# Performance work log

Hardware: AMD Instinct MI355X
Metric: run time of the kernel (lower is better)

## Reference

```python
import jax, jax.numpy as jnp
import numpy as np

HIDDEN = 256
OUT_CH = 3
OMEGA_0 = 30.0
PATCH = 5


def setup_inputs() -> dict:
    key = jax.random.key(0)
    ks = jax.random.split(key, 9)
    B, C, H, W = 1, 128, 256, 256
    in_dim = C * PATCH * PATCH + 2  # 3202
    xi = jax.random.normal(ks[0], (B, C, H, W), dtype=jnp.float32)

    def lin(kw, kb, fi, fo):
        s = 1.0 / np.sqrt(fi)
        Wm = jax.random.uniform(kw, (fi, fo), jnp.float32, -s, s)
        bm = jax.random.uniform(kb, (fo,), jnp.float32, -s, s)
        return Wm, bm

    W1, b1 = lin(ks[1], ks[2], in_dim, HIDDEN)
    W2, b2 = lin(ks[3], ks[4], HIDDEN, HIDDEN)
    W3, b3 = lin(ks[5], ks[6], HIDDEN, HIDDEN)
    W4, b4 = lin(ks[7], ks[8], HIDDEN, OUT_CH)
    return {"xi": xi, "W1": W1, "b1": b1, "W2": W2, "b2": b2,
            "W3": W3, "b3": b3, "W4": W4, "b4": b4}


def _make_coords(B, H, W, dtype):
    # normalized pixel coords in [-1, 1], shape [B*H*W, 2]
    ys = jnp.linspace(-1.0, 1.0, H, dtype=dtype)
    xs = jnp.linspace(-1.0, 1.0, W, dtype=dtype)
    gy, gx = jnp.meshgrid(ys, xs, indexing="ij")
    coords = jnp.stack([gy, gx], axis=-1).reshape(H * W, 2)
    return jnp.tile(coords, (B, 1))


def reference(xi, W1, b1, W2, b2, W3, b3, W4, b4):
    B, C, H, W = xi.shape
    # im2col 5x5 patch gather (zero pad), like F.unfold with padding=2
    patches = jax.lax.conv_general_dilated_patches(
        xi, (PATCH, PATCH), (1, 1), "SAME")  # [B, C*25, H, W]
    feat = jnp.transpose(patches, (0, 2, 3, 1)).reshape(B * H * W, C * PATCH * PATCH)
    coords = _make_coords(B, H, W, xi.dtype)
    x = jnp.concatenate([feat, coords], axis=-1)  # [N, 3202]
    h = jnp.sin(OMEGA_0 * (x @ W1 + b1))
    h = jnp.sin(OMEGA_0 * (h @ W2 + b2))
    h = jnp.sin(OMEGA_0 * (h @ W3 + b3))
    out = h @ W4 + b4  # [N, 3]
    rgb = out.reshape(B, H, W, OUT_CH).transpose(0, 3, 1, 2)
    return rgb
```

## Files before the change

kernel.cpp:

```cpp
#include <hip/hip_runtime.h>
#include <math.h>
#include <stdint.h>

typedef _Float16 f16;
typedef _Float16 f16x8 __attribute__((ext_vector_type(8)));
typedef float f32x4 __attribute__((ext_vector_type(4)));
typedef unsigned short u16;
typedef u16 u16x8 __attribute__((ext_vector_type(8)));

#define HID 256
#define NS1C 100
#define NS2 8
#define NPX 65536
#define BPXG 256
#define NBG (NPX/BPXG)
#define SPAD 260
#define NSP (SPAD*SPAD)

#define OFF_W1C 0
#define SZ_W1C  ((size_t)NS1C*32768)
#define OFF_W2  SZ_W1C
#define SZ_W2   ((size_t)NS2*32768)
#define OFF_W3  (OFF_W2+SZ_W2)
#define OFF_XH  ((size_t)4194304)
#define SZ_XP   ((size_t)NSP*128*2)
#define OFF_XL  (OFF_XH + SZ_XP)
#define OFF_HH  (OFF_XL + SZ_XP)
#define SZ_HP   ((size_t)NPX*HID*2)
#define OFF_HL  (OFF_HH + SZ_HP)

__device__ static const int TAPOFF25[25] = {
  0*SPAD+0, 0*SPAD+1, 0*SPAD+2, 0*SPAD+3, 0*SPAD+4,
  1*SPAD+0, 1*SPAD+1, 1*SPAD+2, 1*SPAD+3, 1*SPAD+4,
  2*SPAD+0, 2*SPAD+1, 2*SPAD+2, 2*SPAD+3, 2*SPAD+4,
  3*SPAD+0, 3*SPAD+1, 3*SPAD+2, 3*SPAD+3, 3*SPAD+4,
  4*SPAD+0, 4*SPAD+1, 4*SPAD+2, 4*SPAD+3, 4*SPAD+4
};

__device__ inline void split2(float v, u16& h, u16& l){
  f16 hv = (f16)v;
  f16 lv = (f16)(v - (float)hv);
  h = __builtin_bit_cast(u16, hv);
  l = __builtin_bit_cast(u16, lv);
}

__device__ inline void prep_w_body(const float* __restrict__ W, int Kact,
                                   u16* __restrict__ outp, int t){
  int s = t >> 10, r = t & 1023;
  int w = r >> 8, nf = (r >> 6) & 3, l = r & 63;
  int col = w*64 + nf*16 + (l & 15);
  int kb  = s*32 + (l >> 4)*8;
  u16x8 hv, lv;
  #pragma unroll
  for (int j = 0; j < 8; ++j){
    int k = kb + j;
    float v = (k < Kact) ? W[(size_t)k*HID + col] : 0.f;
    u16 h, lo; split2(v, h, lo);
    hv[j] = h; lv[j] = lo;
  }
  size_t U0 = ((((size_t)s*4 + w)*4 + nf)*2 + 0)*64 + l;
  *(u16x8*)(outp + U0*8)      = hv;
  *(u16x8*)(outp + (U0+64)*8) = lv;
}

__device__ inline void prep_w1c_body(const float* __restrict__ W1,
                                     u16* __restrict__ outp, int t){
  int s = t >> 10, r = t & 1023;
  int w = r >> 8, nf = (r >> 6) & 3, l = r & 63;
  int col = w*64 + nf*16 + (l & 15);
  int tap = s >> 2, cg = s & 3;
  int cb  = cg*32 + (l >> 4)*8;
  u16x8 hv, lv;
  #pragma unroll
  for (int j = 0; j < 8; ++j){
    int c = cb + j;
    float v = W1[(size_t)(c*25 + tap)*HID + col];
    u16 h, lo; split2(v, h, lo);
    hv[j] = h; lv[j] = lo;
  }
  size_t U0 = ((((size_t)s*4 + w)*4 + nf)*2 + 0)*64 + l;
  *(u16x8*)(outp + U0*8)      = hv;
  *(u16x8*)(outp + (U0+64)*8) = lv;
}

__device__ inline void prep_x_body(const float* __restrict__ xi,
                                   u16* __restrict__ Xh, u16* __restrict__ Xl,
                                   int sp){
  if (sp >= NSP) return;
  int py = sp / SPAD;
  int px = sp - py*SPAD;
  bool inb = (py >= 2) & (py < 258) & (px >= 2) & (px < 258);
  const float* xin = xi + ((size_t)(py-2)<<8) + (px-2);
  #pragma unroll 4
  for (int cg = 0; cg < 16; ++cg){
    u16x8 hv, lv;
    #pragma unroll
    for (int j = 0; j < 8; ++j){
      float v = inb ? xin[((size_t)(cg*8 + j))<<16] : 0.f;
      u16 h, l; split2(v, h, l); hv[j] = h; lv[j] = l;
    }
    *(u16x8*)(Xh + (size_t)sp*128 + cg*8) = hv;
    *(u16x8*)(Xl + (size_t)sp*128 + cg*8) = lv;
  }
}

__global__ __launch_bounds__(256)
void prep_all(const float* __restrict__ xi, const float* __restrict__ W1,
              const float* __restrict__ W2, const float* __restrict__ W3,
              u16* __restrict__ W1c, u16* __restrict__ W2p, u16* __restrict__ W3p,
              u16* __restrict__ Xh, u16* __restrict__ Xl){
  int bid = blockIdx.x, tid = threadIdx.x;
  if (bid < 400){
    prep_w1c_body(W1, W1c, bid*256 + tid);
  } else if (bid < 432){
    prep_w_body(W2, HID, W2p, (bid-400)*256 + tid);
  } else if (bid < 464){
    prep_w_body(W3, HID, W3p, (bid-432)*256 + tid);
  } else {
    prep_x_body(xi, Xh, Xl, (bid-464)*256 + tid);
  }
}

template<int MODE>
__global__ __launch_bounds__(512, 2)
void gemm(const u16* __restrict__ Ah, const u16* __restrict__ Al,
          const u16* __restrict__ Wp, const float* __restrict__ W1,
          const float* __restrict__ bias, u16* __restrict__ Hh, u16* __restrict__ Hl,
          const float* __restrict__ W4, const float* __restrict__ b4,
          float* __restrict__ out, int nt)
{
  __shared__ __align__(16) u16 Sb[65536];

  const int tid  = threadIdx.x;
  const int lane = tid & 63;
  const int wv   = tid >> 6;
  const int wm   = wv >> 2, wn = wv & 3;

  int bid = blockIdx.x;
  bid = (bid & 7)*(NBG/8) + (bid >> 3);
  const int pxb = bid * BPXG;
  const int y   = bid;

  const int ybase  = y*SPAD;
  const int alane  = (lane & 15);
  const int akoff  = (lane >> 4)*8;
  const size_t abase0 = MODE == 0
      ? ((size_t)(ybase + wv*32 + alane)*128 + akoff)
      : ((size_t)(pxb + wv*32 + alane)*HID + akoff);
  const size_t abaseStride = MODE == 0 ? (size_t)16*128 : (size_t)16*HID;

  f32x4 acc[8][4];
  #pragma unroll
  for (int a=0;a<8;a++)
    #pragma unroll
    for (int bq=0;bq<4;bq++) acc[a][bq] = f32x4{0.f,0.f,0.f,0.f};

#define A_STAGE(S, BUF) do { \
    size_t soff; \
    if (MODE == 0){ \
      const int tap = (S) >> 2, cg = (S) & 3; \
      soff = abase0 + (size_t)TAPOFF25[tap]*128 + cg*32; \
    } else { \
      soff = abase0 + (size_t)(S)*32; \
    } \
    _Pragma("unroll") \
    for (int u=0;u<2;++u){ \
      const int mfb = wv*2 + u; \
      const size_t off = soff + (size_t)u*abaseStride; \
      __builtin_amdgcn_global_load_lds( \
        (const __attribute__((address_space(1))) uint32_t*)(Ah + off), \
        (__attribute__((address_space(3))) uint32_t*)((char*)Sb + (size_t)(BUF)*32768 + (mfb*2+0)*1024), \
        16, 0, 0); \
      __builtin_amdgcn_global_load_lds( \
        (const __attribute__((address_space(1))) uint32_t*)(Al + off), \
        (__attribute__((address_space(3))) uint32_t*)((char*)Sb + (size_t)(BUF)*32768 + (mfb*2+1)*1024), \
        16, 0, 0); \
    } \
  } while(0)

#define B_STAGE(S, BUF) do { \
    const char* _src = (const char*)Wp + (size_t)(S)*32768 + wv*4096 + lane*16; \
    char* _dst = (char*)Sb + 65536 + (size_t)(BUF)*32768 + wv*4096; \
    _Pragma("unroll") \
    for (int i=0;i<4;++i) \
      __builtin_amdgcn_global_load_lds( \
        (const __attribute__((address_space(1))) uint32_t*)(_src + i*1024), \
        (__attribute__((address_space(3))) uint32_t*)(_dst + i*1024), 16, 0, 0); \
  } while(0)

  A_STAGE(0, 0); B_STAGE(0, 0);

  for (int t = 0; t < nt; ++t){
    asm volatile("s_waitcnt vmcnt(0)" ::: "memory");
    __builtin_amdgcn_s_barrier();
    __builtin_amdgcn_sched_barrier(0);
    const int cur = t & 1;

    const u16* Abuf = (const u16*)Sb + (size_t)cur*16384;
    const u16* Bbuf = (const u16*)Sb + 32768 + (size_t)cur*16384;

    f16x8 bh[4], bl[4];
    #pragma unroll
    for (int nf=0;nf<4;++nf){
      bh[nf] = *(const f16x8*)(Bbuf + ((size_t)((wn*4+nf)*2+0)*64 + lane)*8);
      bl[nf] = *(const f16x8*)(Bbuf + ((size_t)((wn*4+nf)*2+1)*64 + lane)*8);
    }
    __builtin_amdgcn_sched_barrier(0);
    if (t+1 < nt){
      A_STAGE(t+1, cur^1);
      B_STAGE(t+1, cur^1);
    }

    __builtin_amdgcn_s_setprio(1);
    #pragma unroll
    for (int hf=0; hf<2; ++hf){
      f16x8 ahv[4], alv[4];
      #pragma unroll
      for (int m=0;m<4;++m){
        const int mfb = wm*8 + hf*4 + m;
        ahv[m] = *(const f16x8*)(Abuf + ((size_t)(mfb*2+0)*64 + lane)*8);
        alv[m] = *(const f16x8*)(Abuf + ((size_t)(mfb*2+1)*64 + lane)*8);
      }
      #pragma unroll
      for (int m=0;m<4;++m)
        #pragma unroll
        for (int nf=0;nf<4;++nf)
          acc[hf*4+m][nf] = __builtin_amdgcn_mfma_f32_16x16x32_f16(ahv[m], bh[nf], acc[hf*4+m][nf], 0,0,0);
      #pragma unroll
      for (int m=0;m<4;++m)
        #pragma unroll
        for (int nf=0;nf<4;++nf)
          acc[hf*4+m][nf] = __builtin_amdgcn_mfma_f32_16x16x32_f16(alv[m], bh[nf], acc[hf*4+m][nf], 0,0,0);
      #pragma unroll
      for (int m=0;m<4;++m)
        #pragma unroll
        for (int nf=0;nf<4;++nf)
          acc[hf*4+m][nf] = __builtin_amdgcn_mfma_f32_16x16x32_f16(ahv[m], bl[nf], acc[hf*4+m][nf], 0,0,0);
    }
    __builtin_amdgcn_s_setprio(0);
  }

  __syncthreads();

  float bcol[4];
  #pragma unroll
  for (int nf=0;nf<4;++nf) bcol[nf] = bias[wn*64 + nf*16 + (lane&15)];

  if (MODE == 0){
    float wyv[4], wxv[4];
    #pragma unroll
    for (int nf=0;nf<4;++nf){
      int col = wn*64 + nf*16 + (lane&15);
      wyv[nf] = W1[(size_t)3200*HID + col];
      wxv[nf] = W1[(size_t)3201*HID + col];
    }
    const float gy = -1.f + (2.f/255.f)*(float)y;
    #pragma unroll
    for (int mf=0;mf<8;++mf)
      #pragma unroll
      for (int nf=0;nf<4;++nf)
        #pragma unroll
        for (int j=0;j<4;++j){
          int row = wm*128 + mf*16 + (lane>>4)*4 + j;
          float gx = -1.f + (2.f/255.f)*(float)row;
          float z = acc[mf][nf][j] + bcol[nf] + gy*wyv[nf] + gx*wxv[nf];
          float h = sinf(30.f*z);
          u16 hh,ll; split2(h,hh,ll);
          int col = wn*64 + nf*16 + (lane&15);
          size_t o = (size_t)(pxb+row)*HID + col;
          Hh[o] = hh; Hl[o] = ll;
        }
  } else if (MODE == 1){
    #pragma unroll
    for (int mf=0;mf<8;++mf)
      #pragma unroll
      for (int nf=0;nf<4;++nf)
        #pragma unroll
        for (int j=0;j<4;++j){
          float z = acc[mf][nf][j] + bcol[nf];
          float h = sinf(30.f*z);
          u16 hh,ll; split2(h,hh,ll);
          int row = wm*128 + mf*16 + (lane>>4)*4 + j;
          int col = wn*64 + nf*16 + (lane&15);
          size_t o = (size_t)(pxb+row)*HID + col;
          Hh[o] = hh; Hl[o] = ll;
        }
  } else {
    float (*red)[BPXG][3] = (float(*)[BPXG][3])(void*)Sb;
    float w4v[4][3];
    #pragma unroll
    for (int nf=0;nf<4;++nf){
      int col = wn*64 + nf*16 + (lane&15);
      w4v[nf][0]=W4[col*3+0]; w4v[nf][1]=W4[col*3+1]; w4v[nf][2]=W4[col*3+2];
    }
    #pragma unroll
    for (int mf=0;mf<8;++mf)
      #pragma unroll
      for (int j=0;j<4;++j){
        float s0=0.f,s1=0.f,s2=0.f;
        #pragma unroll
        for (int nf=0;nf<4;++nf){
          float h = sinf(30.f*(acc[mf][nf][j] + bcol[nf]));
          s0 += h*w4v[nf][0]; s1 += h*w4v[nf][1]; s2 += h*w4v[nf][2];
        }
        #pragma unroll
        for (int m=1;m<16;m<<=1){
          s0 += __shfl_xor(s0, m);
          s1 += __shfl_xor(s1, m);
          s2 += __shfl_xor(s2, m);
        }
        if ((lane & 15) == 0){
          int row = wm*128 + mf*16 + (lane>>4)*4 + j;
          red[wn + wm*4][row][0]=s0; red[wn + wm*4][row][1]=s1; red[wn + wm*4][row][2]=s2;
        }
      }
    __syncthreads();
    for (int o = tid; o < BPXG*3; o += 512){
      int px = o & 255, c = o >> 8;
      int wb = (px >> 7)*4;
      float v = red[wb+0][px][c]+red[wb+1][px][c]+red[wb+2][px][c]+red[wb+3][px][c] + b4[c];
      out[(size_t)c*NPX + pxb + px] = v;
    }
  }
#undef A_STAGE
#undef B_STAGE
}

extern "C" void kernel_launch(void* const* d_in, const int* in_sizes, int n_in,
                              void* d_out, int out_size, void* d_ws, size_t ws_size,
                              hipStream_t stream) {
  const float* xi = (const float*)d_in[0];
  const float* W1 = (const float*)d_in[1];
  const float* b1 = (const float*)d_in[2];
  const float* W2 = (const float*)d_in[3];
  const float* b2 = (const float*)d_in[4];
  const float* W3 = (const float*)d_in[5];
  const float* b3 = (const float*)d_in[6];
  const float* W4 = (const float*)d_in[7];
  const float* b4 = (const float*)d_in[8];
  float* out = (float*)d_out;

  char* ws = (char*)d_ws;
  u16* W1c = (u16*)(ws + OFF_W1C);
  u16* W2p = (u16*)(ws + OFF_W2);
  u16* W3p = (u16*)(ws + OFF_W3);
  u16* Xh  = (u16*)(ws + OFF_XH);
  u16* Xl  = (u16*)(ws + OFF_XL);
  u16* Hh  = (u16*)(ws + OFF_HH);
  u16* Hl  = (u16*)(ws + OFF_HL);

  prep_all<<<729, 256, 0, stream>>>(xi, W1, W2, W3, W1c, W2p, W3p, Xh, Xl);

  dim3 grid(NBG), block(512);
  gemm<0><<<grid, block, 0, stream>>>(Xh, Xl, W1c, W1, b1, Hh, Hl,
                                      nullptr, nullptr, nullptr, NS1C);
  gemm<1><<<grid, block, 0, stream>>>(Hh, Hl, W2p, nullptr, b2, Hh, Hl,
                                      nullptr, nullptr, nullptr, NS2);
  gemm<2><<<grid, block, 0, stream>>>(Hh, Hl, W3p, nullptr, b3, nullptr, nullptr,
                                      W4, b4, out, NS2);
}
```

Before: 457.4 us.

## Split GEMM K-step into barrier-separated phases interleaving LDS reads, prefetch and MFMA clusters

Restructures the inner GEMM loop into six phases. Each phase loads a small set of A/B fragments from LDS, issues part of the next-stage global-to-LDS prefetch (A in phase one, B in phase two), then runs a 4x4 MFMA cluster at raised priority. Workgroup barriers separate the phases. The goal is a ping-pong schedule in which waves overlap LDS reads and MFMA work, and register pressure drops because fewer fragments are live at once. The cost is many extra s_barriers per K-step, which can stall waves and hurt throughput.

```diff
diff --git a/kernel.cpp b/kernel.cpp
--- a/kernel.cpp
+++ b/kernel.cpp
@@ -141,11 +141,10 @@
   const int pxb = bid * BPXG;
   const int y   = bid;
 
-  const int ybase  = y*SPAD;
   const int alane  = (lane & 15);
   const int akoff  = (lane >> 4)*8;
   const size_t abase0 = MODE == 0
-      ? ((size_t)(ybase + wv*32 + alane)*128 + akoff)
+      ? ((size_t)(y*SPAD + wv*32 + alane)*128 + akoff)
       : ((size_t)(pxb + wv*32 + alane)*HID + akoff);
   const size_t abaseStride = MODE == 0 ? (size_t)16*128 : (size_t)16*HID;
 
@@ -188,6 +187,29 @@
         (__attribute__((address_space(3))) uint32_t*)(_dst + i*1024), 16, 0, 0); \
   } while(0)
 
+#define CLUSTER(AV, BV, BASE) do { \
+    __builtin_amdgcn_s_setprio(1); \
+    _Pragma("unroll") \
+    for (int m=0;m<4;++m) \
+      _Pragma("unroll") \
+      for (int nf=0;nf<4;++nf) \
+        acc[(BASE)+m][nf] = __builtin_amdgcn_mfma_f32_16x16x32_f16(AV[m], BV[nf], acc[(BASE)+m][nf], 0,0,0); \
+    __builtin_amdgcn_s_setprio(0); \
+  } while(0)
+
+#define PHASE_BAR() do { \
+    __builtin_amdgcn_sched_barrier(0); \
+    __builtin_amdgcn_s_barrier(); \
+    asm volatile("s_waitcnt lgkmcnt(0)" ::: "memory"); \
+    __builtin_amdgcn_sched_barrier(0); \
+  } while(0)
+
+#define POST_BAR() do { \
+    __builtin_amdgcn_sched_barrier(0); \
+    __builtin_amdgcn_s_barrier(); \
+    __builtin_amdgcn_sched_barrier(0); \
+  } while(0)
+
   A_STAGE(0, 0); B_STAGE(0, 0);
 
   for (int t = 0; t < nt; ++t){
@@ -199,45 +221,52 @@
     const u16* Abuf = (const u16*)Sb + (size_t)cur*16384;
     const u16* Bbuf = (const u16*)Sb + 32768 + (size_t)cur*16384;
 
-    f16x8 bh[4], bl[4];
-    #pragma unroll
-    for (int nf=0;nf<4;++nf){
+    f16x8 bh[4], a0h[4];
+    #pragma unroll
+    for (int nf=0;nf<4;++nf)
       bh[nf] = *(const f16x8*)(Bbuf + ((size_t)((wn*4+nf)*2+0)*64 + lane)*8);
+    #pragma unroll
+    for (int m=0;m<4;++m)
+      a0h[m] = *(const f16x8*)(Abuf + ((size_t)((wm*8+m)*2+0)*64 + lane)*8);
+    if (t+1 < nt) A_STAGE(t+1, cur^1);
+    PHASE_BAR();
+    CLUSTER(a0h, bh, 0);
+    POST_BAR();
+
+    f16x8 a0l[4];
+    #pragma unroll
+    for (int m=0;m<4;++m)
+      a0l[m] = *(const f16x8*)(Abuf + ((size_t)((wm*8+m)*2+1)*64 + lane)*8);
+    if (t+1 < nt) B_STAGE(t+1, cur^1);
+    PHASE_BAR();
+    CLUSTER(a0l, bh, 0);
+    POST_BAR();
+
+    f16x8 bl[4];
+    #pragma unroll
+    for (int nf=0;nf<4;++nf)
       bl[nf] = *(const f16x8*)(Bbuf + ((size_t)((wn*4+nf)*2+1)*64 + lane)*8);
-    }
-    __builtin_amdgcn_sched_barrier(0);
-    if (t+1 < nt){
-      A_STAGE(t+1, cur^1);
-      B_STAGE(t+1, cur^1);
-    }
-
-    __builtin_amdgcn_s_setprio(1);
-    #pragma unroll
-    for (int hf=0; hf<2; ++hf){
-      f16x8 ahv[4], alv[4];
-      #pragma unroll
-      for (int m=0;m<4;++m){
-        const int mfb = wm*8 + hf*4 + m;
-        ahv[m] = *(const f16x8*)(Abuf + ((size_t)(mfb*2+0)*64 + lane)*8);
-        alv[m] = *(const f16x8*)(Abuf + ((size_t)(mfb*2+1)*64 + lane)*8);
-      }
-      #pragma unroll
-      for (int m=0;m<4;++m)
-        #pragma unroll
-        for (int nf=0;nf<4;++nf)
-          acc[hf*4+m][nf] = __builtin_amdgcn_mfma_f32_16x16x32_f16(ahv[m], bh[nf], acc[hf*4+m][nf], 0,0,0);
-      #pragma unroll
-      for (int m=0;m<4;++m)
-        #pragma unroll
-        for (int nf=0;nf<4;++nf)
-          acc[hf*4+m][nf] = __builtin_amdgcn_mfma_f32_16x16x32_f16(alv[m], bh[nf], acc[hf*4+m][nf], 0,0,0);
-      #pragma unroll
-      for (int m=0;m<4;++m)
-        #pragma unroll
-        for (int nf=0;nf<4;++nf)
-          acc[hf*4+m][nf] = __builtin_amdgcn_mfma_f32_16x16x32_f16(ahv[m], bl[nf], acc[hf*4+m][nf], 0,0,0);
-    }
-    __builtin_amdgcn_s_setprio(0);
+    PHASE_BAR();
+    CLUSTER(a0h, bl, 0);
+    POST_BAR();
+
+    f16x8 a1h[4];
+    #pragma unroll
+    for (int m=0;m<4;++m)
+      a1h[m] = *(const f16x8*)(Abuf + ((size_t)((wm*8+4+m)*2+0)*64 + lane)*8);
+    PHASE_BAR();
+    CLUSTER(a1h, bh, 4);
+    POST_BAR();
+
+    f16x8 a1l[4];
+    #pragma unroll
+    for (int m=0;m<4;++m)
+      a1l[m] = *(const f16x8*)(Abuf + ((size_t)((wm*8+4+m)*2+1)*64 + lane)*8);
+    PHASE_BAR();
+    CLUSTER(a1l, bh, 4);
+    POST_BAR();
+
+    CLUSTER(a1h, bl, 4);
   }
 
   __syncthreads();
@@ -324,6 +353,9 @@
   }
 #undef A_STAGE
 #undef B_STAGE
+#undef CLUSTER
+#undef PHASE_BAR
+#undef POST_BAR
 }
 
 extern "C" void kernel_launch(void* const* d_in, const int* in_sizes, int n_in,
```

Measured after the change: 480.1 us. 1.05x slower.
